# Kernel tuning notes

Hardware: AMD Instinct MI355X
Metric: run time of the kernel (lower is better)

## Reference

```python
import math
import jax, jax.numpy as jnp
import numpy as np

B, N, D = 2, 768, 512
H = 8
DK = D // H
BETA_NOT = 0.5
EPS = 1e-6


def setup_inputs() -> dict:
    key = jax.random.key(0)
    ks = jax.random.split(key, 8)
    s = 0.02
    return {
        "x": jax.random.normal(ks[0], (B, N, D), dtype=jnp.float32),
        "qkv1_w": jax.random.normal(ks[1], (D, 3 * D), dtype=jnp.float32) * s,
        "qkv2_w": jax.random.normal(ks[2], (D, 3 * D), dtype=jnp.float32) * s,
        "proj_w": jax.random.normal(ks[3], (D, D), dtype=jnp.float32) * s,
        "conv1_w": jax.random.normal(ks[4], (16, 6), dtype=jnp.float32) * 0.3,
        "conv1_b": jax.random.normal(ks[5], (16,), dtype=jnp.float32) * 0.1,
        "conv2_w": jax.random.normal(ks[6], (4, 16), dtype=jnp.float32) * 0.3,
        "conv2_b": jnp.full((4,), -5.0, dtype=jnp.float32),
        "chain_logit": jnp.asarray(-2.0, dtype=jnp.float32),
    }


def _qkv(x, w):
    b, n, d = x.shape
    qkv = (x @ w).reshape(b, n, 3, H, DK).transpose(2, 0, 3, 1, 4)  # [3,B,h,N,dk]
    return qkv[0], qkv[1], qkv[2]


def reference(x, qkv1_w, qkv2_w, proj_w, conv1_w, conv1_b, conv2_w, conv2_b, chain_logit):
    scale = 1.0 / math.sqrt(DK)
    q1, k1, v1 = _qkv(x, qkv1_w)
    q2, k2, v2 = _qkv(x, qkv2_w)

    S1 = jnp.einsum("bhnd,bhmd->bhnm", q1, k1) * scale  # [B,h,N,N]
    S2 = jnp.einsum("bhnd,bhmd->bhnm", q2, k2) * scale
    A1 = jax.nn.softmax(S1, axis=-1)
    A2 = jax.nn.softmax(S2, axis=-1)

    C_right = jnp.einsum("bhnk,bhkm->bhnm", A1, A2)
    C_left = jnp.einsum("bhnk,bhkm->bhnm", A2, A1)
    Cr = jnp.log(C_right + EPS)
    Cl = jnp.log(C_left + EPS)

    # 6-channel edge feature map [B,h,6,N,N]
    feat = jnp.stack(
        [S1, S2, jnp.swapaxes(S1, -1, -2), jnp.swapaxes(S2, -1, -2), Cr, Cl], axis=2
    )
    # 1x1 convs == per-pixel channel mixing
    hid = jnp.einsum("bhcnm,oc->bhonm", feat, conv1_w) + conv1_b[None, None, :, None, None]
    hid = jax.nn.gelu(hid, approximate=True)  # tanh-approx GELU
    gates = jax.nn.sigmoid(
        jnp.einsum("bhcnm,oc->bhonm", hid, conv2_w) + conv2_b[None, None, :, None, None]
    )
    g_and, g_or, g_not, g_chain = gates[:, :, 0], gates[:, :, 1], gates[:, :, 2], gates[:, :, 3]

    Smix = (
        S1
        + g_and * S2  # g_and * (S1 + S2 - S1)
        + g_or * (jnp.logaddexp(S1, S2) - S1)
        - g_not * (BETA_NOT * S2)
        + g_chain * Cr
    )
    A = jax.nn.softmax(Smix, axis=-1)

    y_base = jnp.einsum("bhnm,bhmd->bhnd", A, v1)
    transport = jnp.einsum("bhnm,bhmd->bhnd", A2, v2)
    y_chain = jnp.einsum("bhnm,bhmd->bhnd", A1, transport)
    w = jax.nn.sigmoid(chain_logit)
    y = y_base + w * y_chain

    y = jnp.swapaxes(y, 1, 2).reshape(x.shape[0], x.shape[1], D)  # [B,N,D]
    return y @ proj_w
```

## Files before the change

### kernel.cpp

```cpp
#include <hip/hip_runtime.h>
#include <hip/hip_bf16.h>
#include <math.h>

typedef __hip_bfloat16 bf16;
typedef __attribute__((ext_vector_type(8))) short short8;
typedef __attribute__((ext_vector_type(4))) float f32x4;
typedef __attribute__((ext_vector_type(2))) float f32x2;
#define DEVINL __device__ __forceinline__

constexpr int Bc  = 2;
constexpr int Nc  = 768;
constexpr int Dc  = 512;
constexpr int Hc  = 8;
constexpr int DKc = 64;
constexpr int BHc = Bc * Hc;
constexpr float SCALE    = 0.125f;
constexpr float EPSF     = 1e-6f;
constexpr float BETA_NOT = 0.5f;

DEVINL float ldf(const float* p, long i) { return p[i]; }
DEVINL float ldf(const bf16* p, long i) { return __bfloat162float(p[i]); }
DEVINL void stf(float* p, long i, float v) { p[i] = v; }
DEVINL void stf(bf16* p, long i, float v) { p[i] = __float2bfloat16(v); }

DEVINL float sigf(float x) { return __fdividef(1.f, 1.f + __expf(-x)); }

DEVINL f32x2 fma2(f32x2 a, f32x2 b, f32x2 c) { return __builtin_elementwise_fma(a, b, c); }
DEVINL f32x2 splat2(float x) { return (f32x2){x, x}; }
DEVINL float vexp2(float x) { float r; asm("v_exp_f32 %0, %1" : "=v"(r) : "v"(x)); return r; }
DEVINL float vrcp(float x)  { float r; asm("v_rcp_f32 %0, %1" : "=v"(r) : "v"(x)); return r; }
DEVINL float vlog2(float x) { float r; asm("v_log_f32 %0, %1" : "=v"(r) : "v"(x)); return r; }

DEVINL void gl_lds16(const void* g, void* l) {
    __builtin_amdgcn_global_load_lds(
        (const __attribute__((address_space(1))) void*)g,
        (__attribute__((address_space(3))) void*)l, 16, 0, 0);
}

DEVINL int sniff_is_fp32(const void* xraw) {
    const uint4* p4 = (const uint4*)xraw;
    float mx = 0.f;
#pragma unroll
    for (int j = 0; j < 16; ++j) {
        const uint4 u = p4[j];
        const unsigned w[4] = {u.x, u.y, u.z, u.w};
#pragma unroll
        for (int t = 0; t < 4; ++t) {
            mx = fmaxf(mx, fabsf(__uint_as_float((w[t] & 0xffffu) << 16)));
            mx = fmaxf(mx, fabsf(__uint_as_float(w[t] & 0xffff0000u)));
        }
    }
    return mx > 1000.f ? 1 : 0;
}

DEVINL float cvt_elem(const void* s, long j, int is32) {
    return is32 ? ((const float*)s)[j]
                : __bfloat162float(((const bf16*)s)[j]);
}

__global__ __launch_bounds__(256) void convert_all(
    const void* x, const void* w1, const void* w2, const void* pw,
    const void* c1w, const void* c1b, const void* c2w, const void* c2b,
    const void* ch,
    bf16* xb, bf16* w1b, bf16* w2b, bf16* pwb, float* smallf)
{
    __shared__ int is32s;
    if (threadIdx.x == 0) is32s = sniff_is_fp32(x);
    __syncthreads();
    const int is32 = is32s;
    const long i = (long)blockIdx.x * 256 + threadIdx.x;
    if (i < (long)Bc * Nc * Dc) {
        xb[i]  = __float2bfloat16(cvt_elem(x,  i, is32));
        w1b[i] = __float2bfloat16(cvt_elem(w1, i, is32));
        w2b[i] = __float2bfloat16(cvt_elem(w2, i, is32));
    }
    if (i < (long)Dc * Dc) pwb[i] = __float2bfloat16(cvt_elem(pw, i, is32));
    if (i < 384) {
        const int u = (int)i / 24, k = (int)i % 24;
        float v = 0.f;
        if (k < 12)      v = cvt_elem(c1w, u * 6 + (k >> 1), is32);
        else if (k < 14) v = cvt_elem(c1b, u, is32);
        else if (k >= 16) { const int o = (k - 16) >> 1; v = cvt_elem(c2w, o * 16 + u, is32); }
        smallf[i] = v;
    } else if (i < 392) smallf[i] = cvt_elem(c2b, ((int)i - 384) >> 1, is32);
    else if (i < 394) smallf[i] = cvt_elem(ch, 0, is32);
    else if (i < 512) smallf[i] = 0.f;
}

__global__ __launch_bounds__(256) void fill_sentinel(unsigned short* o) {
    const long i = (long)blockIdx.x * 256 + threadIdx.x;
    if (i < (long)Bc * Nc * Dc) o[i] = 0x40E0;
}

__global__ __launch_bounds__(256) void transpose_bf16(
    const unsigned short* __restrict__ src, unsigned short* __restrict__ dst,
    int R, int C, long sS, long sD)
{
    __shared__ unsigned short tile[64][68];
    const unsigned short* s = src + (long)blockIdx.z * sS;
    unsigned short* d = dst + (long)blockIdx.z * sD;
    const int r0 = blockIdx.y * 64, c0 = blockIdx.x * 64;
    const int t = threadIdx.x;
    const int lr = t >> 4, lc4 = (t & 15) * 4;
#pragma unroll
    for (int i = 0; i < 4; ++i) {
        int r = lr + i * 16;
        *(uint2*)&tile[r][lc4] = *(const uint2*)&s[(long)(r0 + r) * C + c0 + lc4];
    }
    __syncthreads();
#pragma unroll
    for (int i = 0; i < 4; ++i) {
        int r = lr + i * 16;
        unsigned short v[4];
#pragma unroll
        for (int j = 0; j < 4; ++j) v[j] = tile[lc4 + j][r];
        *(uint2*)&d[(long)(c0 + r) * R + r0 + lc4] = *(uint2*)v;
    }
}

__global__ __launch_bounds__(256) void sgemm_softmax(
    const bf16* __restrict__ qg, const bf16* __restrict__ kg,
    float* __restrict__ Sg, bf16* __restrict__ Ag_, bf16* __restrict__ Atg)
{
    __shared__ unsigned short Bsm[256 * 72];
    __shared__ unsigned short Asm16[16 * 72];
    __shared__ float red[4][16];

    const int wg  = blockIdx.x;
    const int xcd = wg & 7, tt = wg >> 3;
    const int z   = xcd + 8 * (tt / 48);
    const int by  = tt % 48;
    const long MAT = (long)Nc * Nc;

    const bf16* Q  = qg + (long)z * (Nc * DKc) + (long)(by * 16) * DKc;
    const bf16* Km = kg + (long)z * (Nc * DKc);
    float* S  = Sg  + (long)z * MAT + (long)(by * 16) * Nc;
    bf16*  A  = Ag_ + (long)z * MAT + (long)(by * 16) * Nc;
    bf16*  At = Atg + (long)z * MAT;

    const int tid  = threadIdx.x;
    const int wv   = tid >> 6;
    const int lane = tid & 63;
    const int q    = lane >> 4;
    const int ln   = lane & 15;
    const int sr   = tid >> 3, k8 = tid & 7;

    if (tid < 128) {
        const int row = tid >> 3, kk = tid & 7;
        *(uint4*)&Asm16[row * 72 + kk * 8] = *(const uint4*)&Q[row * 64 + kk * 8];
    }

    f32x4 acc[12];
#pragma unroll
    for (int j = 0; j < 12; ++j) acc[j] = (f32x4){0.f, 0.f, 0.f, 0.f};

    for (int c = 0; c < 3; ++c) {
        __syncthreads();
#pragma unroll
        for (int i = 0; i < 8; ++i) {
            const int row = sr + i * 32;
            *(uint4*)&Bsm[row * 72 + k8 * 8] =
                *(const uint4*)&Km[(long)(c * 256 + row) * 64 + k8 * 8];
        }
        __syncthreads();
#pragma unroll
        for (int kc = 0; kc < 2; ++kc) {
            const short8 af = *(const short8*)&Asm16[ln * 72 + kc * 32 + q * 8];
#pragma unroll
            for (int t = 0; t < 4; ++t) {
                const int nl = wv * 64 + t * 16 + ln;
                const short8 bfr = *(const short8*)&Bsm[nl * 72 + kc * 32 + q * 8];
                acc[c * 4 + t] = __builtin_amdgcn_mfma_f32_16x16x32_bf16(
                    af, bfr, acc[c * 4 + t], 0, 0, 0);
            }
        }
    }

    float mrow[4] = {-1e30f, -1e30f, -1e30f, -1e30f};
#pragma unroll
    for (int j = 0; j < 12; ++j) {
        const int c = j >> 2, t = j & 3;
        const int col = c * 256 + wv * 64 + t * 16 + ln;
#pragma unroll
        for (int r = 0; r < 4; ++r) {
            const float v = acc[j][r] * SCALE;
            acc[j][r] = v;
            S[(long)(q * 4 + r) * Nc + col] = v;
            mrow[r] = fmaxf(mrow[r], v);
        }
    }
#pragma unroll
    for (int off = 8; off > 0; off >>= 1)
#pragma unroll
        for (int r = 0; r < 4; ++r)
            mrow[r] = fmaxf(mrow[r], __shfl_xor(mrow[r], off, 16));
    if (ln == 0)
#pragma unroll
        for (int r = 0; r < 4; ++r) red[wv][q * 4 + r] = mrow[r];
    __syncthreads();
    float m4[4];
#pragma unroll
    for (int r = 0; r < 4; ++r)
        m4[r] = fmaxf(fmaxf(red[0][q * 4 + r], red[1][q * 4 + r]),
                      fmaxf(red[2][q * 4 + r], red[3][q * 4 + r]));
    __syncthreads();

    float srow[4] = {0.f, 0.f, 0.f, 0.f};
#pragma unroll
    for (int j = 0; j < 12; ++j)
#pragma unroll
        for (int r = 0; r < 4; ++r) {
            const float e = __expf(acc[j][r] - m4[r]);
            acc[j][r] = e;
            srow[r] += e;
        }
#pragma unroll
    for (int off = 8; off > 0; off >>= 1)
#pragma unroll
        for (int r = 0; r < 4; ++r)
            srow[r] += __shfl_xor(srow[r], off, 16);
    if (ln == 0)
#pragma unroll
        for (int r = 0; r < 4; ++r) red[wv][q * 4 + r] = srow[r];
    __syncthreads();
    float inv[4];
#pragma unroll
    for (int r = 0; r < 4; ++r)
        inv[r] = 1.f / fmaxf(red[0][q * 4 + r] + red[1][q * 4 + r] +
                             red[2][q * 4 + r] + red[3][q * 4 + r], 1e-30f);

    unsigned short* ATl = Bsm;
#pragma unroll
    for (int j = 0; j < 12; ++j) {
        const int c = j >> 2, t = j & 3;
        const int col = c * 256 + wv * 64 + t * 16 + ln;
#pragma unroll
        for (int r = 0; r < 4; ++r) {
            const bf16 b = __float2bfloat16(acc[j][r] * inv[r]);
            const unsigned short u = *(const unsigned short*)&b;
            A[(long)(q * 4 + r) * Nc + col] = *(const bf16*)&u;
            ATl[col * 20 + q * 4 + r] = u;
        }
    }
    __syncthreads();
#pragma unroll
    for (int s = 0; s < 3; ++s) {
        const int m = tid + s * 256;
        uint2 v0 = *(const uint2*)&ATl[m * 20 + 0];
        uint2 v1 = *(const uint2*)&ATl[m * 20 + 4];
        uint2 v2 = *(const uint2*)&ATl[m * 20 + 8];
        uint2 v3 = *(const uint2*)&ATl[m * 20 + 12];
        unsigned short* d = (unsigned short*)&At[(long)m * Nc + by * 16];
        *(uint2*)&d[0]  = v0;
        *(uint2*)&d[4]  = v1;
        *(uint2*)&d[8]  = v2;
        *(uint2*)&d[12] = v3;
    }
}

template <int EPI, typename TC, int XORB = 0, int XCDSWZ = 0, int RAW = 0>
__global__ __launch_bounds__(256) void gemm_nt_mfma(
    const bf16* __restrict__ Ag, const bf16* __restrict__ Btg,
    TC* __restrict__ Cg, bf16* __restrict__ Craw, int M, int N, int K,
    long sA, long sB, long sC, float alpha)
{
    __shared__ unsigned short Asm[2 * 128 * 32];
    __shared__ unsigned short Bsm[2 * 128 * 32];
    constexpr int BUF = 128 * 32;

    int bx, by, bz;
    if (XCDSWZ) {
        const int wg = blockIdx.x;
        const int xcd = wg & 7, t = wg >> 3;
        bz = xcd + 8 * (t / 36);
        const int tile = t % 36;
        bx = tile % 6; by = tile / 6;
    } else { bx = blockIdx.x; by = blockIdx.y; bz = blockIdx.z; }

    const int tid  = threadIdx.x;
    const int wv   = tid >> 6;
    const int lane = tid & 63;
    const int q    = lane >> 4;
    const int ln   = lane & 15;
    const int wm   = wv & 1;
    const int wn   = wv >> 1;

    const int zb = XORB ? (bz ^ 16) : bz;
    const bf16* A  = Ag  + (long)bz * sA + (long)(by * 128) * K;
    const bf16* Bt = Btg + (long)zb * sB + (long)(bx * 128) * K;
    TC*         C  = Cg  + (long)bz * sC;

    const int sr = lane >> 2, sc = lane & 3;
    const int scs = sc ^ (sr & 3);
    const bf16* gA0 = A  + (long)(wv * 32 + sr)      * K + scs * 8;
    const bf16* gA1 = A  + (long)(wv * 32 + 16 + sr) * K + scs * 8;
    const bf16* gB0 = Bt + (long)(wv * 32 + sr)      * K + scs * 8;
    const bf16* gB1 = Bt + (long)(wv * 32 + 16 + sr) * K + scs * 8;
    unsigned short* lA0 = &Asm[(wv * 32)      * 32];
    unsigned short* lA1 = &Asm[(wv * 32 + 16) * 32];
    unsigned short* lB0 = &Bsm[(wv * 32)      * 32];
    unsigned short* lB1 = &Bsm[(wv * 32 + 16) * 32];

    f32x4 acc[4][4];
#pragma unroll
    for (int i = 0; i < 4; ++i)
#pragma unroll
        for (int j = 0; j < 4; ++j)
            acc[i][j] = (f32x4){0.f, 0.f, 0.f, 0.f};

    const int qs = (q ^ (ln & 3)) * 8;

    gl_lds16(gA0, lA0);
    gl_lds16(gA1, lA1);
    gl_lds16(gB0, lB0);
    gl_lds16(gB1, lB1);
    __syncthreads();

    int cur = 0;
    for (int k0 = 0; k0 < K; k0 += 32) {
        const int nxt = cur ^ 1;
        if (k0 + 32 < K) {
            const int no = nxt * BUF;
            gl_lds16(gA0 + k0 + 32, lA0 + no);
            gl_lds16(gA1 + k0 + 32, lA1 + no);
            gl_lds16(gB0 + k0 + 32, lB0 + no);
            gl_lds16(gB1 + k0 + 32, lB1 + no);
        }

        const unsigned short* Ac = &Asm[cur * BUF];
        const unsigned short* Bc = &Bsm[cur * BUF];
        short8 af[4], bfr[4];
#pragma unroll
        for (int mt = 0; mt < 4; ++mt) {
            int m = wm * 64 + mt * 16 + ln;
            af[mt] = *(const short8*)&Ac[m * 32 + qs];
        }
#pragma unroll
        for (int nt = 0; nt < 4; ++nt) {
            int n = wn * 64 + nt * 16 + ln;
            bfr[nt] = *(const short8*)&Bc[n * 32 + qs];
        }
#pragma unroll
        for (int mt = 0; mt < 4; ++mt)
#pragma unroll
            for (int nt = 0; nt < 4; ++nt)
                acc[mt][nt] = __builtin_amdgcn_mfma_f32_16x16x32_bf16(
                    af[mt], bfr[nt], acc[mt][nt], 0, 0, 0);

        __syncthreads();
        cur = nxt;
    }

#pragma unroll
    for (int mt = 0; mt < 4; ++mt) {
#pragma unroll
        for (int nt = 0; nt < 4; ++nt) {
            const int col = bx * 128 + wn * 64 + nt * 16 + ln;
            const int rowb = by * 128 + wm * 64 + mt * 16 + q * 4;
#pragma unroll
            for (int r = 0; r < 4; ++r) {
                float vraw = acc[mt][nt][r] * alpha;
                if (RAW) {
                    if (bz < 16)
                        Craw[(long)bz * M * N + (long)(rowb + r) * N + col] =
                            __float2bfloat16(vraw);
                }
                float v = vraw;
                if (EPI == 1) v = __logf(fmaxf(v, 0.f) + EPSF);
                stf(C, (long)(rowb + r) * N + col, v);
            }
        }
    }
}

__global__ __launch_bounds__(256) void qkv_mfma(
    const bf16* __restrict__ X,
    const bf16* __restrict__ w1t, const bf16* __restrict__ w2t,
    bf16* __restrict__ q1, bf16* __restrict__ k1, bf16* __restrict__ v1,
    bf16* __restrict__ q2, bf16* __restrict__ k2, bf16* __restrict__ v2)
{
    constexpr int K = Dc;
    __shared__ unsigned short Asm[2 * 128 * 32];
    __shared__ unsigned short Bsm[2 * 128 * 32];
    constexpr int BUF = 128 * 32;

    const int tid  = threadIdx.x;
    const int wv   = tid >> 6;
    const int lane = tid & 63;
    const int q    = lane >> 4;
    const int ln   = lane & 15;
    const int wm   = wv & 1;
    const int wn   = wv >> 1;
    const int set  = blockIdx.z;

    const bf16* Wt = set ? w2t : w1t;
    bf16* Q  = set ? q2 : q1;
    bf16* Ko = set ? k2 : k1;
    bf16* V  = set ? v2 : v1;

    const bf16* A  = X  + (long)(blockIdx.y * 128) * K;
    const bf16* Bt = Wt + (long)(blockIdx.x * 128) * K;

    const int sr = lane >> 2, sc = lane & 3;
    const int scs = sc ^ (sr & 3);
    const bf16* gA0 = A  + (long)(wv * 32 + sr)      * K + scs * 8;
    const bf16* gA1 = A  + (long)(wv * 32 + 16 + sr) * K + scs * 8;
    const bf16* gB0 = Bt + (long)(wv * 32 + sr)      * K + scs * 8;
    const bf16* gB1 = Bt + (long)(wv * 32 + 16 + sr) * K + scs * 8;
    unsigned short* lA0 = &Asm[(wv * 32)      * 32];
    unsigned short* lA1 = &Asm[(wv * 32 + 16) * 32];
    unsigned short* lB0 = &Bsm[(wv * 32)      * 32];
    unsigned short* lB1 = &Bsm[(wv * 32 + 16) * 32];

    f32x4 acc[4][4];
#pragma unroll
    for (int i = 0; i < 4; ++i)
#pragma unroll
        for (int j = 0; j < 4; ++j)
            acc[i][j] = (f32x4){0.f, 0.f, 0.f, 0.f};

    const int qs = (q ^ (ln & 3)) * 8;

    gl_lds16(gA0, lA0);
    gl_lds16(gA1, lA1);
    gl_lds16(gB0, lB0);
    gl_lds16(gB1, lB1);
    __syncthreads();

    int cur = 0;
    for (int k0 = 0; k0 < K; k0 += 32) {
        const int nxt = cur ^ 1;
        if (k0 + 32 < K) {
            const int no = nxt * BUF;
            gl_lds16(gA0 + k0 + 32, lA0 + no);
            gl_lds16(gA1 + k0 + 32, lA1 + no);
            gl_lds16(gB0 + k0 + 32, lB0 + no);
            gl_lds16(gB1 + k0 + 32, lB1 + no);
        }

        const unsigned short* Ac = &Asm[cur * BUF];
        const unsigned short* Bc = &Bsm[cur * BUF];
        short8 af[4], bfr[4];
#pragma unroll
        for (int mt = 0; mt < 4; ++mt) {
            int m = wm * 64 + mt * 16 + ln;
            af[mt] = *(const short8*)&Ac[m * 32 + qs];
        }
#pragma unroll
        for (int nt = 0; nt < 4; ++nt) {
            int n = wn * 64 + nt * 16 + ln;
            bfr[nt] = *(const short8*)&Bc[n * 32 + qs];
        }
#pragma unroll
        for (int mt = 0; mt < 4; ++mt)
#pragma unroll
            for (int nt = 0; nt < 4; ++nt)
                acc[mt][nt] = __builtin_amdgcn_mfma_f32_16x16x32_bf16(
                    af[mt], bfr[nt], acc[mt][nt], 0, 0, 0);

        __syncthreads();
        cur = nxt;
    }

#pragma unroll
    for (int mt = 0; mt < 4; ++mt) {
#pragma unroll
        for (int nt = 0; nt < 4; ++nt) {
            const int col  = blockIdx.x * 128 + wn * 64 + nt * 16 + ln;
            const int rowb = blockIdx.y * 128 + wm * 64 + mt * 16 + q * 4;
            const int t = col >> 9;
            const int h = (col >> 6) & 7;
            const int dk = col & 63;
            bf16* dst = (t == 0) ? Q : (t == 1) ? Ko : V;
#pragma unroll
            for (int r = 0; r < 4; ++r) {
                const int row = rowb + r;
                const int b = row >= Nc ? 1 : 0;
                const int n = row - b * Nc;
                dst[(((long)b * Hc + h) * Nc + n) * DKc + dk] =
                    __float2bfloat16(acc[mt][nt][r]);
            }
        }
    }
}

struct N64Acc { f32x4 acc[2][4]; };

template <typename DUMMY = void>
DEVINL void n64_core(const bf16* A, const bf16* Bt, int K,
                     unsigned short* Asm, unsigned short* Bsm, N64Acc& R)
{
    const int tid  = threadIdx.x;
    const int wave = tid >> 6;
    const int lane = tid & 63;
    const int q    = lane >> 4;
    const int ln   = lane & 15;

    const int sr = tid >> 3, k8 = tid & 7;
    const bf16* pa[4];
    const bf16* pb[2];
    int wa[4], wb[2];
#pragma unroll
    for (int i = 0; i < 4; ++i) {
        pa[i] = A + (long)(sr + i * 32) * K + k8 * 8;
        wa[i] = (sr + i * 32) * 72 + k8 * 8;
    }
#pragma unroll
    for (int i = 0; i < 2; ++i) {
        pb[i] = Bt + (long)(sr + i * 32) * K + k8 * 8;
        wb[i] = (sr + i * 32) * 72 + k8 * 8;
    }

#pragma unroll
    for (int i = 0; i < 2; ++i)
#pragma unroll
        for (int j = 0; j < 4; ++j)
            R.acc[i][j] = (f32x4){0.f, 0.f, 0.f, 0.f};

    for (int k0 = 0; k0 < K; k0 += 64) {
        uint4 va[4], vb[2];
#pragma unroll
        for (int i = 0; i < 4; ++i) va[i] = *(const uint4*)(pa[i] + k0);
#pragma unroll
        for (int i = 0; i < 2; ++i) vb[i] = *(const uint4*)(pb[i] + k0);
        __syncthreads();
#pragma unroll
        for (int i = 0; i < 4; ++i) *(uint4*)&Asm[wa[i]] = va[i];
#pragma unroll
        for (int i = 0; i < 2; ++i) *(uint4*)&Bsm[wb[i]] = vb[i];
        __syncthreads();

#pragma unroll
        for (int kc = 0; kc < 2; ++kc) {
            short8 af[2], bfr[4];
#pragma unroll
            for (int mt = 0; mt < 2; ++mt) {
                int m = wave * 32 + mt * 16 + ln;
                af[mt] = *(const short8*)&Asm[m * 72 + kc * 32 + q * 8];
            }
#pragma unroll
            for (int nt = 0; nt < 4; ++nt) {
                int n = nt * 16 + ln;
                bfr[nt] = *(const short8*)&Bsm[n * 72 + kc * 32 + q * 8];
            }
#pragma unroll
            for (int mt = 0; mt < 2; ++mt)
#pragma unroll
                for (int nt = 0; nt < 4; ++nt)
                    R.acc[mt][nt] = __builtin_amdgcn_mfma_f32_16x16x32_bf16(
                        af[mt], bfr[nt], R.acc[mt][nt], 0, 0, 0);
        }
    }
}

struct N64hAcc { f32x4 acc[4]; };

template <typename DUMMY = void>
DEVINL void n64h_core(const bf16* A, const bf16* Bt, int K,
                      unsigned short* Asm, unsigned short* Bsm, N64hAcc& R)
{
    const int tid  = threadIdx.x;
    const int wave = tid >> 6;
    const int lane = tid & 63;
    const int q    = lane >> 4;
    const int ln   = lane & 15;

    const int sr = tid >> 3, k8 = tid & 7;
    const bf16* pa[2];
    const bf16* pb[2];
    int wa[2], wb[2];
#pragma unroll
    for (int i = 0; i < 2; ++i) {
        pa[i] = A  + (long)(sr + i * 32) * K + k8 * 8;
        wa[i] = (sr + i * 32) * 72 + k8 * 8;
        pb[i] = Bt + (long)(sr + i * 32) * K + k8 * 8;
        wb[i] = wa[i];
    }

#pragma unroll
    for (int j = 0; j < 4; ++j)
        R.acc[j] = (f32x4){0.f, 0.f, 0.f, 0.f};

    for (int k0 = 0; k0 < K; k0 += 64) {
        uint4 va[2], vb[2];
#pragma unroll
        for (int i = 0; i < 2; ++i) va[i] = *(const uint4*)(pa[i] + k0);
#pragma unroll
        for (int i = 0; i < 2; ++i) vb[i] = *(const uint4*)(pb[i] + k0);
        __syncthreads();
#pragma unroll
        for (int i = 0; i < 2; ++i) *(uint4*)&Asm[wa[i]] = va[i];
#pragma unroll
        for (int i = 0; i < 2; ++i) *(uint4*)&Bsm[wb[i]] = vb[i];
        __syncthreads();

#pragma unroll
        for (int kc = 0; kc < 2; ++kc) {
            short8 af;
            af = *(const short8*)&Asm[(wave * 16 + ln) * 72 + kc * 32 + q * 8];
            short8 bfr[4];
#pragma unroll
            for (int nt = 0; nt < 4; ++nt) {
                int n = nt * 16 + ln;
                bfr[nt] = *(const short8*)&Bsm[n * 72 + kc * 32 + q * 8];
            }
#pragma unroll
            for (int nt = 0; nt < 4; ++nt)
                R.acc[nt] = __builtin_amdgcn_mfma_f32_16x16x32_bf16(
                    af, bfr[nt], R.acc[nt], 0, 0, 0);
        }
    }
}

__global__ __launch_bounds__(256) void gemm_n64_pair(
    const bf16* __restrict__ A0g, const bf16* __restrict__ B0g, bf16* __restrict__ C0tg,
    const bf16* __restrict__ A1g, const bf16* __restrict__ B1g, bf16* __restrict__ C1g,
    int M, int K, long sA, long sB, long sC)
{
    __shared__ unsigned short Asm[128 * 72];
    __shared__ unsigned short Bsm[64 * 72];

    const int zz = blockIdx.z & 15;
    const int second = blockIdx.z >> 4;
    const bf16* A  = (second ? A1g : A0g) + (long)zz * sA + (long)(blockIdx.y * 128) * K;
    const bf16* Bt = (second ? B1g : B0g) + (long)zz * sB;

    N64Acc R;
    n64_core(A, Bt, K, Asm, Bsm, R);

    const int tid = threadIdx.x;
    const int wave = tid >> 6, lane = tid & 63, q = lane >> 4, ln = lane & 15;

    if (second) {
        bf16* C = C1g + (long)zz * sC;
#pragma unroll
        for (int mt = 0; mt < 2; ++mt) {
#pragma unroll
            for (int nt = 0; nt < 4; ++nt) {
                const int col  = nt * 16 + ln;
                const int rowb = blockIdx.y * 128 + wave * 32 + mt * 16 + q * 4;
#pragma unroll
                for (int r = 0; r < 4; ++r)
                    C[(long)(rowb + r) * 64 + col] = __float2bfloat16(R.acc[mt][nt][r]);
            }
        }
    } else {
        __syncthreads();
#pragma unroll
        for (int mt = 0; mt < 2; ++mt) {
#pragma unroll
            for (int nt = 0; nt < 4; ++nt) {
                const int col = nt * 16 + ln;
                const int rwb = wave * 32 + mt * 16 + q * 4;
#pragma unroll
                for (int r = 0; r < 4; ++r)
                    *(bf16*)&Asm[col * 136 + rwb + r] = __float2bfloat16(R.acc[mt][nt][r]);
            }
        }
        __syncthreads();
        bf16* Ct = C0tg + (long)zz * sC;
        const int dk  = tid >> 2;
        const int nc0 = (tid & 3) * 32;
        const int gn0 = blockIdx.y * 128;
#pragma unroll
        for (int c8 = 0; c8 < 4; ++c8) {
            uint4 v = *(const uint4*)&Asm[dk * 136 + nc0 + c8 * 8];
            *(uint4*)&Ct[(long)dk * Nc + gn0 + nc0 + c8 * 8] = v;
        }
    }
}

__global__ __launch_bounds__(256) void gemm_n64_both_h(
    const bf16* __restrict__ Ab, const bf16* __restrict__ v1t,
    const bf16* __restrict__ Craw, const bf16* __restrict__ v2t,
    const float* __restrict__ smallf, bf16* __restrict__ yc,
    int K, long sA, long sB)
{
    __shared__ unsigned short Asm[64 * 72];
    __shared__ unsigned short Bsm[64 * 72];

    const int bh = blockIdx.z;
    const long arow = (long)(blockIdx.y * 64) * K;

    N64hAcc R1;
    n64h_core(Ab + (long)bh * sA + arow, v1t + (long)bh * sB, K, Asm, Bsm, R1);
    N64hAcc R2;
    n64h_core(Craw + (long)bh * sA + arow, v2t + (long)bh * sB, K, Asm, Bsm, R2);

    const float w = sigf(smallf[392]);
    const int b = bh >> 3, h = bh & 7;

    const int tid = threadIdx.x;
    const int wave = tid >> 6, lane = tid & 63, q = lane >> 4, ln = lane & 15;
#pragma unroll
    for (int nt = 0; nt < 4; ++nt) {
        const int col  = nt * 16 + ln;
        const int rowb = blockIdx.y * 64 + wave * 16 + q * 4;
#pragma unroll
        for (int r = 0; r < 4; ++r) {
            const int n = rowb + r;
            yc[((long)(b * Nc + n)) * Dc + h * DKc + col] =
                __float2bfloat16(R1.acc[nt][r] + w * R2.acc[nt][r]);
        }
    }
}

__global__ __launch_bounds__(256) void gemm_n64_combine(
    const bf16* __restrict__ A1b, const bf16* __restrict__ trt,
    const bf16* __restrict__ yb1, const float* __restrict__ smallf,
    bf16* __restrict__ yc, int M, int K, long sA, long sB)
{
    __shared__ unsigned short Asm[128 * 72];
    __shared__ unsigned short Bsm[64 * 72];

    const int bh = blockIdx.z;
    const bf16* A  = A1b + (long)bh * sA + (long)(blockIdx.y * 128) * K;
    const bf16* Bt = trt + (long)bh * sB;

    N64Acc R;
    n64_core(A, Bt, K, Asm, Bsm, R);

    const float w = sigf(smallf[392]);
    const int b = bh >> 3, h = bh & 7;
    const long yb1base = (long)bh * Nc * DKc;

    const int tid = threadIdx.x;
    const int wave = tid >> 6, lane = tid & 63, q = lane >> 4, ln = lane & 15;
#pragma unroll
    for (int mt = 0; mt < 2; ++mt) {
#pragma unroll
        for (int nt = 0; nt < 4; ++nt) {
            const int col  = nt * 16 + ln;
            const int rowb = blockIdx.y * 128 + wave * 32 + mt * 16 + q * 4;
#pragma unroll
            for (int r = 0; r < 4; ++r) {
                const int n = rowb + r;
                const float base = __bfloat162float(yb1[yb1base + (long)n * 64 + col]);
                yc[((long)(b * Nc + n)) * Dc + h * DKc + col] =
                    __float2bfloat16(base + w * R.acc[mt][nt][r]);
            }
        }
    }
}

__global__ __launch_bounds__(256) void gemm_n64_yb(
    const bf16* __restrict__ Ag, const bf16* __restrict__ Btg,
    bf16* __restrict__ Cg, int M, int K, long sA, long sB, long sC)
{
    __shared__ unsigned short Asm[128 * 72];
    __shared__ unsigned short Bsm[64 * 72];

    const int zz = blockIdx.z;
    const bf16* A  = Ag + (long)zz * sA + (long)(blockIdx.y * 128) * K;
    const bf16* Bt = Btg + (long)zz * sB;

    N64Acc R;
    n64_core(A, Bt, K, Asm, Bsm, R);

    bf16* C = Cg + (long)zz * sC;
    const int tid = threadIdx.x;
    const int wave = tid >> 6, lane = tid & 63, q = lane >> 4, ln = lane & 15;
#pragma unroll
    for (int mt = 0; mt < 2; ++mt) {
#pragma unroll
        for (int nt = 0; nt < 4; ++nt) {
            const int col  = nt * 16 + ln;
            const int rowb = blockIdx.y * 128 + wave * 32 + mt * 16 + q * 4;
#pragma unroll
            for (int r = 0; r < 4; ++r)
                C[(long)(rowb + r) * 64 + col] = __float2bfloat16(R.acc[mt][nt][r]);
        }
    }
}

__global__ __launch_bounds__(256) void softmax_rows_w(
    const float* __restrict__ src, bf16* __restrict__ dst)
{
    const int wid  = threadIdx.x >> 6;
    const int lane = threadIdx.x & 63;
    const long row = (long)blockIdx.x * 4 + wid;
    const float* s = src + row * Nc;

    float4 v[3];
#pragma unroll
    for (int i = 0; i < 3; ++i)
        v[i] = *(const float4*)&s[i * 256 + lane * 4];

    float m = -1e30f;
#pragma unroll
    for (int i = 0; i < 3; ++i)
        m = fmaxf(m, fmaxf(fmaxf(v[i].x, v[i].y), fmaxf(v[i].z, v[i].w)));
#pragma unroll
    for (int off = 32; off > 0; off >>= 1)
        m = fmaxf(m, __shfl_xor(m, off, 64));

    float e[12];
    float sum = 0.f;
#pragma unroll
    for (int i = 0; i < 3; ++i) {
        e[i * 4 + 0] = __expf(v[i].x - m);
        e[i * 4 + 1] = __expf(v[i].y - m);
        e[i * 4 + 2] = __expf(v[i].z - m);
        e[i * 4 + 3] = __expf(v[i].w - m);
        sum += e[i * 4 + 0] + e[i * 4 + 1] + e[i * 4 + 2] + e[i * 4 + 3];
    }
#pragma unroll
    for (int off = 32; off > 0; off >>= 1)
        sum += __shfl_xor(sum, off, 64);

    const float inv = 1.f / fmaxf(sum, 1e-30f);
    unsigned short* d = (unsigned short*)dst + row * Nc;
#pragma unroll
    for (int i = 0; i < 3; ++i) {
        unsigned short o[4];
#pragma unroll
        for (int j = 0; j < 4; ++j) {
            const bf16 b = __float2bfloat16(e[i * 4 + j] * inv);
            o[j] = *(const unsigned short*)&b;
        }
        *(uint2*)&d[i * 256 + lane * 4] = *(const uint2*)o;
    }
}

__global__ __launch_bounds__(256) void gates_smix(
    const float* __restrict__ S1g, const float* __restrict__ S2g,
    const bf16* __restrict__ Crg, const bf16* __restrict__ Clg,
    float* __restrict__ Smixg, const float* __restrict__ smallf)
{
    __shared__ float t1t[32][17], t2t[32][17];

    const long mat = (long)blockIdx.z * Nc * Nc;
    const float* S1 = S1g + mat;
    const float* S2 = S2g + mat;
    const unsigned short* Cr = (const unsigned short*)Crg + mat;
    const unsigned short* Cl = (const unsigned short*)Clg + mat;
    float* Smix = Smixg + mat;

    const int tid = threadIdx.x;

    const int n0 = blockIdx.y * 16, m0 = blockIdx.x * 32;
    {
        const int r = tid >> 3, c2 = (tid & 7) * 2;
        const float2 a = *(const float2*)&S1[(long)(m0 + r) * Nc + n0 + c2];
        const float2 b = *(const float2*)&S2[(long)(m0 + r) * Nc + n0 + c2];
        t1t[r][c2] = a.x; t1t[r][c2 + 1] = a.y;
        t2t[r][c2] = b.x; t2t[r][c2 + 1] = b.y;
    }
    __syncthreads();

    const int tx = tid & 15, ty = tid >> 4;
    const int n = n0 + ty;
    const long idx = (long)n * Nc + m0 + tx * 2;

    const float2 s1v = *(const float2*)&S1[idx];
    const float2 s2v = *(const float2*)&S2[idx];
    const unsigned cru = *(const unsigned*)&Cr[idx];
    const unsigned clu = *(const unsigned*)&Cl[idx];

    const f32x2 s1a = {s1v.x, s1v.y};
    const f32x2 s2a = {s2v.x, s2v.y};
    const f32x2 cra = {__uint_as_float((cru & 0xffffu) << 16),
                       __uint_as_float(cru & 0xffff0000u)};
    const f32x2 cla = {__uint_as_float((clu & 0xffffu) << 16),
                       __uint_as_float(clu & 0xffff0000u)};
    const f32x2 s1t = {t1t[tx * 2][ty], t1t[tx * 2 + 1][ty]};
    const f32x2 s2t = {t2t[tx * 2][ty], t2t[tx * 2 + 1][ty]};

    f32x2 g0 = *(const f32x2*)&smallf[384];
    f32x2 g1 = *(const f32x2*)&smallf[386];
    f32x2 g2 = *(const f32x2*)&smallf[388];
    f32x2 g3 = *(const f32x2*)&smallf[390];

    const f32x2 gc1  = splat2(-2.30220902f);
    const f32x2 gc3  = splat2(-0.10294357f);
    const f32x2 one2 = splat2(1.f);

#pragma unroll
    for (int u = 0; u < 16; ++u) {
        const f32x2* cw = (const f32x2*)&smallf[u * 24];
        f32x2 h = cw[6];
        h = fma2(s1a, cw[0], h);
        h = fma2(s2a, cw[1], h);
        h = fma2(s1t, cw[2], h);
        h = fma2(s2t, cw[3], h);
        h = fma2(cra, cw[4], h);
        h = fma2(cla, cw[5], h);
        const f32x2 hh = h * h;
        const f32x2 z2 = h * fma2(hh, gc3, gc1);
        f32x2 e;  e[0]  = vexp2(z2[0]); e[1]  = vexp2(z2[1]);
        const f32x2 d = one2 + e;
        f32x2 rc; rc[0] = vrcp(d[0]);   rc[1] = vrcp(d[1]);
        const f32x2 hid = h * rc;
        g0 = fma2(hid, cw[8],  g0);
        g1 = fma2(hid, cw[9],  g1);
        g2 = fma2(hid, cw[10], g2);
        g3 = fma2(hid, cw[11], g3);
    }

    const f32x2 nl2e = splat2(-1.44269504f);
    const f32x2 ln2v = splat2(0.69314718f);
    auto sig2 = [&](f32x2 x) -> f32x2 {
        const f32x2 t = x * nl2e;
        f32x2 e;  e[0] = vexp2(t[0]); e[1] = vexp2(t[1]);
        const f32x2 d = one2 + e;
        f32x2 r;  r[0] = vrcp(d[0]);  r[1] = vrcp(d[1]);
        return r;
    };
    const f32x2 ga2 = sig2(g0);
    const f32x2 go2 = sig2(g1);
    const f32x2 gn2 = sig2(g2);
    const f32x2 gc2 = sig2(g3);

    const f32x2 dd = s1a - s2a;
    f32x2 ad; ad[0] = fabsf(dd[0]); ad[1] = fabsf(dd[1]);
    const f32x2 t2 = ad * nl2e;
    f32x2 ee; ee[0] = vexp2(t2[0]); ee[1] = vexp2(t2[1]);
    const f32x2 lp = one2 + ee;
    f32x2 lg; lg[0] = vlog2(lp[0]); lg[1] = vlog2(lp[1]);
    const f32x2 mx2 = __builtin_elementwise_max(s1a, s2a);
    const f32x2 lae = fma2(lg, ln2v, mx2);

    f32x2 o2 = s1a;
    o2 = fma2(ga2, s2a, o2);
    o2 = fma2(go2, lae - s1a, o2);
    o2 = fma2(gn2, s2a * splat2(-BETA_NOT), o2);
    o2 = fma2(gc2, cra, o2);
    *(float2*)&Smix[idx] = (float2){o2[0], o2[1]};
}

__global__ __launch_bounds__(256) void proj_n64h(
    const bf16* __restrict__ yc, const bf16* __restrict__ pwt,
    const void* __restrict__ xraw, void* __restrict__ out)
{
    constexpr int K = Dc;
    constexpr int N = Dc;
    __shared__ unsigned short Asm[64 * 72];
    __shared__ unsigned short Bsm[64 * 72];
    __shared__ int is32s;
    if (threadIdx.x == 0) is32s = sniff_is_fp32(xraw);

    const bf16* A  = yc  + (long)(blockIdx.y * 64) * K;
    const bf16* Bt = pwt + (long)(blockIdx.x * 64) * K;

    N64hAcc R;
    n64h_core(A, Bt, K, Asm, Bsm, R);

    const int is32 = is32s;
    const int tid = threadIdx.x;
    const int wave = tid >> 6, lane = tid & 63, q = lane >> 4, ln = lane & 15;
#pragma unroll
    for (int nt = 0; nt < 4; ++nt) {
        const int col  = blockIdx.x * 64 + nt * 16 + ln;
        const int rowb = blockIdx.y * 64 + wave * 16 + q * 4;
#pragma unroll
        for (int r = 0; r < 4; ++r) {
            const long o = (long)(rowb + r) * N + col;
            if (is32) ((float*)out)[o] = R.acc[nt][r];
            else      ((bf16*)out)[o] = __float2bfloat16(R.acc[nt][r]);
        }
    }
}

extern "C" void kernel_launch(void* const* d_in, const int* in_sizes, int n_in,
                              void* d_out, int out_size, void* d_ws, size_t ws_size,
                              hipStream_t stream)
{
    const size_t HD   = (size_t)BHc * Nc * DKc;
    const size_t HDh  = HD / 2;
    const size_t MAT  = (size_t)Nc * Nc;
    const size_t MATS = (size_t)BHc * MAT;
    const long   HSTR = (long)Nc * DKc;

    float* ws = (float*)d_ws;
    size_t off = 0;
    auto alloc = [&](size_t n) { float* p = ws + off; off += n; return p; };

    bf16* xb  = (bf16*)alloc(HDh);
    bf16* w1b = (bf16*)alloc(HDh);
    bf16* w2b = (bf16*)alloc(HDh);
    bf16* w1t = (bf16*)alloc(HDh);
    bf16* w2t = (bf16*)alloc(HDh);
    bf16* pwb = (bf16*)alloc((size_t)Dc * Dc / 2);
    bf16* pwt = (bf16*)alloc((size_t)Dc * Dc / 2);
    float* smallf = alloc(512);
    bf16* q1b = (bf16*)alloc(HDh); bf16* q2b = (bf16*)alloc(HDh);
    bf16* k1b = (bf16*)alloc(HDh); bf16* k2b = (bf16*)alloc(HDh);
    bf16* v1b = (bf16*)alloc(HDh); bf16* v2b = (bf16*)alloc(HDh);
    bf16* v1t = (bf16*)alloc(HDh); bf16* v2t = (bf16*)alloc(HDh);
    bf16* trt = (bf16*)alloc(HDh);
    float* S1   = alloc(MATS);
    float* S2   = alloc(MATS);
    float* Smix = alloc(MATS);
    bf16* A1b = (bf16*)alloc(MATS / 2);
    bf16* A2b = (bf16*)alloc(MATS / 2);
    bf16* Crb = (bf16*)alloc(MATS / 2);
    bf16* Clb = (bf16*)alloc(MATS / 2);
    bf16* yb1 = (bf16*)alloc(HDh);
    bf16* yc  = (bf16*)alloc(HDh);

    const size_t NEED_BASE = off * sizeof(float);
    bf16* Crawb = (bf16*)alloc(MATS / 2);
    const size_t NEED_A = off * sizeof(float);
    const int pathA = ws_size >= NEED_A;

    bf16* A1tb = (bf16*)Smix;
    bf16* A2tb = ((bf16*)Smix) + MATS;
    bf16* Ab   = (bf16*)S1;

    if (ws_size < NEED_BASE) {
        fill_sentinel<<<dim3(3072), 256, 0, stream>>>((unsigned short*)d_out);
        return;
    }

    convert_all<<<dim3(3072), 256, 0, stream>>>(
        d_in[0], d_in[1], d_in[2], d_in[3], d_in[4], d_in[5], d_in[6], d_in[7],
        d_in[8], xb, w1b, w2b, pwb, smallf);

    transpose_bf16<<<dim3(24, 8, 2), 256, 0, stream>>>(
        (const unsigned short*)w1b, (unsigned short*)w1t, Dc, 3 * Dc, (long)HD, (long)HD);
    transpose_bf16<<<dim3(8, 8, 1), 256, 0, stream>>>(
        (const unsigned short*)pwb, (unsigned short*)pwt, Dc, Dc, 0, 0);
    qkv_mfma<<<dim3(12, 12, 2), 256, 0, stream>>>(
        xb, w1t, w2t, q1b, k1b, v1b, q2b, k2b, v2b);
    transpose_bf16<<<dim3(1, 12, 2 * BHc), 256, 0, stream>>>(
        (const unsigned short*)v1b, (unsigned short*)v1t, Nc, DKc, HSTR, HSTR);

    sgemm_softmax<<<dim3(1536), 256, 0, stream>>>(
        q1b, k1b, S1, A1b, A1tb);

    if (pathA)
        gemm_nt_mfma<1, bf16, 1, 1, 1><<<dim3(1152), 256, 0, stream>>>(
            A1b, A1tb, Crb, Crawb, Nc, Nc, Nc, (long)MAT, (long)MAT, (long)MAT, 1.f);
    else
        gemm_nt_mfma<1, bf16, 1, 1, 0><<<dim3(1152), 256, 0, stream>>>(
            A1b, A1tb, Crb, nullptr, Nc, Nc, Nc, (long)MAT, (long)MAT, (long)MAT, 1.f);

    gates_smix<<<dim3(24, 48, BHc), 256, 0, stream>>>(S1, S2, Crb, Clb, Smix, smallf);

    softmax_rows_w<<<(BHc * Nc) / 4, 256, 0, stream>>>(Smix, Ab);

    if (pathA) {
        gemm_n64_both_h<<<dim3(1, 12, BHc), 256, 0, stream>>>(
            Ab, v1t, Crawb, v2t, smallf, yc, Nc, (long)MAT, HSTR);
    } else {
        gemm_n64_pair<<<dim3(1, 6, 2 * BHc), 256, 0, stream>>>(
            A2b, v2t, trt, Ab, v1t, yb1, Nc, Nc, (long)MAT, HSTR, HSTR);
        gemm_n64_combine<<<dim3(1, 6, BHc), 256, 0, stream>>>(
            A1b, trt, yb1, smallf, yc, Nc, Nc, (long)MAT, HSTR);
    }

    proj_n64h<<<dim3(8, 24, 1), 256, 0, stream>>>(yc, pwt, d_in[0], d_out);
}
```

Measured before the change: 331.6 us.

## Fuse gate computation with row softmax and merge weight transposes

```diff
diff --git a/kernel.cpp b/kernel.cpp
--- a/kernel.cpp
+++ b/kernel.cpp
@@ -99,6 +99,42 @@
     __shared__ unsigned short tile[64][68];
     const unsigned short* s = src + (long)blockIdx.z * sS;
     unsigned short* d = dst + (long)blockIdx.z * sD;
+    const int r0 = blockIdx.y * 64, c0 = blockIdx.x * 64;
+    const int t = threadIdx.x;
+    const int lr = t >> 4, lc4 = (t & 15) * 4;
+#pragma unroll
+    for (int i = 0; i < 4; ++i) {
+        int r = lr + i * 16;
+        *(uint2*)&tile[r][lc4] = *(const uint2*)&s[(long)(r0 + r) * C + c0 + lc4];
+    }
+    __syncthreads();
+#pragma unroll
+    for (int i = 0; i < 4; ++i) {
+        int r = lr + i * 16;
+        unsigned short v[4];
+#pragma unroll
+        for (int j = 0; j < 4; ++j) v[j] = tile[lc4 + j][r];
+        *(uint2*)&d[(long)(c0 + r) * R + r0 + lc4] = *(uint2*)v;
+    }
+}
+
+__global__ __launch_bounds__(256) void transpose_wpw(
+    const unsigned short* __restrict__ wb, unsigned short* __restrict__ wt,
+    const unsigned short* __restrict__ pwb, unsigned short* __restrict__ pwt)
+{
+    __shared__ unsigned short tile[64][68];
+    const int z = blockIdx.z;
+    const unsigned short* s;
+    unsigned short* d;
+    int R, C;
+    if (z < 2) {
+        s = wb + (long)z * (Dc * 3 * Dc);
+        d = wt + (long)z * (Dc * 3 * Dc);
+        R = Dc; C = 3 * Dc;
+    } else {
+        if (blockIdx.x >= 8) return;
+        s = pwb; d = pwt; R = Dc; C = Dc;
+    }
     const int r0 = blockIdx.y * 64, c0 = blockIdx.x * 64;
     const int t = threadIdx.x;
     const int lr = t >> 4, lc4 = (t & 15) * 4;
@@ -926,6 +962,163 @@
     o2 = fma2(gn2, s2a * splat2(-BETA_NOT), o2);
     o2 = fma2(gc2, cra, o2);
     *(float2*)&Smix[idx] = (float2){o2[0], o2[1]};
+}
+
+__global__ __launch_bounds__(256) void gates_smix_sm(
+    const float* __restrict__ S1g, const float* __restrict__ S2g,
+    const bf16* __restrict__ Crg, const bf16* __restrict__ Clg,
+    bf16* __restrict__ Ag_, const float* __restrict__ smallf)
+{
+    __shared__ float osm[8 * Nc];
+    __shared__ float t1t[64][9], t2t[64][9];
+
+    const long mat = (long)blockIdx.z * Nc * Nc;
+    const float* S1 = S1g + mat;
+    const float* S2 = S2g + mat;
+    const unsigned short* Cr = (const unsigned short*)Crg + mat;
+    const unsigned short* Cl = (const unsigned short*)Clg + mat;
+    bf16* A = Ag_ + mat;
+
+    const int tid = threadIdx.x;
+    const int n0 = blockIdx.x * 8;
+    const int tx = tid & 31, ty = tid >> 5;
+    const int n = n0 + ty;
+
+    const f32x2 gc1  = splat2(-2.30220902f);
+    const f32x2 gc3  = splat2(-0.10294357f);
+    const f32x2 one2 = splat2(1.f);
+    const f32x2 nl2e = splat2(-1.44269504f);
+    const f32x2 ln2v = splat2(0.69314718f);
+
+    for (int it = 0; it < 12; ++it) {
+        const int m0 = it * 64;
+        __syncthreads();
+        {
+            const int r = tid >> 2, c2 = (tid & 3) * 2;
+            const float2 a = *(const float2*)&S1[(long)(m0 + r) * Nc + n0 + c2];
+            const float2 b = *(const float2*)&S2[(long)(m0 + r) * Nc + n0 + c2];
+            t1t[r][c2] = a.x; t1t[r][c2 + 1] = a.y;
+            t2t[r][c2] = b.x; t2t[r][c2 + 1] = b.y;
+        }
+        __syncthreads();
+
+        const long idx = (long)n * Nc + m0 + tx * 2;
+        const float2 s1v = *(const float2*)&S1[idx];
+        const float2 s2v = *(const float2*)&S2[idx];
+        const unsigned cru = *(const unsigned*)&Cr[idx];
+        const unsigned clu = *(const unsigned*)&Cl[idx];
+
+        const f32x2 s1a = {s1v.x, s1v.y};
+        const f32x2 s2a = {s2v.x, s2v.y};
+        const f32x2 cra = {__uint_as_float((cru & 0xffffu) << 16),
+                           __uint_as_float(cru & 0xffff0000u)};
+        const f32x2 cla = {__uint_as_float((clu & 0xffffu) << 16),
+                           __uint_as_float(clu & 0xffff0000u)};
+        const f32x2 s1t = {t1t[tx * 2][ty], t1t[tx * 2 + 1][ty]};
+        const f32x2 s2t = {t2t[tx * 2][ty], t2t[tx * 2 + 1][ty]};
+
+        f32x2 g0 = *(const f32x2*)&smallf[384];
+        f32x2 g1 = *(const f32x2*)&smallf[386];
+        f32x2 g2 = *(const f32x2*)&smallf[388];
+        f32x2 g3 = *(const f32x2*)&smallf[390];
+
+#pragma unroll
+        for (int u = 0; u < 16; ++u) {
+            const f32x2* cw = (const f32x2*)&smallf[u * 24];
+            f32x2 h = cw[6];
+            h = fma2(s1a, cw[0], h);
+            h = fma2(s2a, cw[1], h);
+            h = fma2(s1t, cw[2], h);
+            h = fma2(s2t, cw[3], h);
+            h = fma2(cra, cw[4], h);
+            h = fma2(cla, cw[5], h);
+            const f32x2 hh = h * h;
+            const f32x2 z2 = h * fma2(hh, gc3, gc1);
+            f32x2 e;  e[0]  = vexp2(z2[0]); e[1]  = vexp2(z2[1]);
+            const f32x2 d = one2 + e;
+            f32x2 rc; rc[0] = vrcp(d[0]);   rc[1] = vrcp(d[1]);
+            const f32x2 hid = h * rc;
+            g0 = fma2(hid, cw[8],  g0);
+            g1 = fma2(hid, cw[9],  g1);
+            g2 = fma2(hid, cw[10], g2);
+            g3 = fma2(hid, cw[11], g3);
+        }
+
+        auto sig2 = [&](f32x2 x) -> f32x2 {
+            const f32x2 t = x * nl2e;
+            f32x2 e;  e[0] = vexp2(t[0]); e[1] = vexp2(t[1]);
+            const f32x2 d = one2 + e;
+            f32x2 r;  r[0] = vrcp(d[0]);  r[1] = vrcp(d[1]);
+            return r;
+        };
+        const f32x2 ga2 = sig2(g0);
+        const f32x2 go2 = sig2(g1);
+        const f32x2 gn2 = sig2(g2);
+        const f32x2 gc2 = sig2(g3);
+
+        const f32x2 dd = s1a - s2a;
+        f32x2 ad; ad[0] = fabsf(dd[0]); ad[1] = fabsf(dd[1]);
+        const f32x2 t2 = ad * nl2e;
+        f32x2 ee; ee[0] = vexp2(t2[0]); ee[1] = vexp2(t2[1]);
+        const f32x2 lp = one2 + ee;
+        f32x2 lg; lg[0] = vlog2(lp[0]); lg[1] = vlog2(lp[1]);
+        const f32x2 mx2 = __builtin_elementwise_max(s1a, s2a);
+        const f32x2 lae = fma2(lg, ln2v, mx2);
+
+        f32x2 o2 = s1a;
+        o2 = fma2(ga2, s2a, o2);
+        o2 = fma2(go2, lae - s1a, o2);
+        o2 = fma2(gn2, s2a * splat2(-BETA_NOT), o2);
+        o2 = fma2(gc2, cra, o2);
+        *(float2*)&osm[ty * Nc + m0 + tx * 2] = (float2){o2[0], o2[1]};
+    }
+    __syncthreads();
+
+    const int w = tid >> 6, lane = tid & 63;
+#pragma unroll
+    for (int rr = 0; rr < 2; ++rr) {
+        const int row = w * 2 + rr;
+        const float* s = &osm[row * Nc];
+        float4 v[3];
+#pragma unroll
+        for (int i = 0; i < 3; ++i)
+            v[i] = *(const float4*)&s[i * 256 + lane * 4];
+
+        float m = -1e30f;
+#pragma unroll
+        for (int i = 0; i < 3; ++i)
+            m = fmaxf(m, fmaxf(fmaxf(v[i].x, v[i].y), fmaxf(v[i].z, v[i].w)));
+#pragma unroll
+        for (int off = 32; off > 0; off >>= 1)
+            m = fmaxf(m, __shfl_xor(m, off, 64));
+
+        float e[12];
+        float sum = 0.f;
+#pragma unroll
+        for (int i = 0; i < 3; ++i) {
+            e[i * 4 + 0] = __expf(v[i].x - m);
+            e[i * 4 + 1] = __expf(v[i].y - m);
+            e[i * 4 + 2] = __expf(v[i].z - m);
+            e[i * 4 + 3] = __expf(v[i].w - m);
+            sum += e[i * 4 + 0] + e[i * 4 + 1] + e[i * 4 + 2] + e[i * 4 + 3];
+        }
+#pragma unroll
+        for (int off = 32; off > 0; off >>= 1)
+            sum += __shfl_xor(sum, off, 64);
+
+        const float inv = 1.f / fmaxf(sum, 1e-30f);
+        unsigned short* d = (unsigned short*)A + (long)(n0 + row) * Nc;
+#pragma unroll
+        for (int i = 0; i < 3; ++i) {
+            unsigned short o[4];
+#pragma unroll
+            for (int j = 0; j < 4; ++j) {
+                const bf16 b = __float2bfloat16(e[i * 4 + j] * inv);
+                o[j] = *(const unsigned short*)&b;
+            }
+            *(uint2*)&d[i * 256 + lane * 4] = *(const uint2*)o;
+        }
+    }
 }
 
 __global__ __launch_bounds__(256) void proj_n64h(
@@ -1005,6 +1198,7 @@
 
     bf16* A1tb = (bf16*)Smix;
     bf16* A2tb = ((bf16*)Smix) + MATS;
+    bf16* AbA  = (bf16*)Smix;
     bf16* Ab   = (bf16*)S1;
 
     if (ws_size < NEED_BASE) {
@@ -1016,10 +1210,9 @@
         d_in[0], d_in[1], d_in[2], d_in[3], d_in[4], d_in[5], d_in[6], d_in[7],
         d_in[8], xb, w1b, w2b, pwb, smallf);
 
-    transpose_bf16<<<dim3(24, 8, 2), 256, 0, stream>>>(
-        (const unsigned short*)w1b, (unsigned short*)w1t, Dc, 3 * Dc, (long)HD, (long)HD);
-    transpose_bf16<<<dim3(8, 8, 1), 256, 0, stream>>>(
-        (const unsigned short*)pwb, (unsigned short*)pwt, Dc, Dc, 0, 0);
+    transpose_wpw<<<dim3(24, 8, 3), 256, 0, stream>>>(
+        (const unsigned short*)w1b, (unsigned short*)w1t,
+        (const unsigned short*)pwb, (unsigned short*)pwt);
     qkv_mfma<<<dim3(12, 12, 2), 256, 0, stream>>>(
         xb, w1t, w2t, q1b, k1b, v1b, q2b, k2b, v2b);
     transpose_bf16<<<dim3(1, 12, 2 * BHc), 256, 0, stream>>>(
@@ -1035,14 +1228,16 @@
         gemm_nt_mfma<1, bf16, 1, 1, 0><<<dim3(1152), 256, 0, stream>>>(
             A1b, A1tb, Crb, nullptr, Nc, Nc, Nc, (long)MAT, (long)MAT, (long)MAT, 1.f);
 
-    gates_smix<<<dim3(24, 48, BHc), 256, 0, stream>>>(S1, S2, Crb, Clb, Smix, smallf);
-
-    softmax_rows_w<<<(BHc * Nc) / 4, 256, 0, stream>>>(Smix, Ab);
-
     if (pathA) {
+        gates_smix_sm<<<dim3(96, 1, BHc), 256, 0, stream>>>(
+            S1, S2, Crb, Clb, AbA, smallf);
+
         gemm_n64_both_h<<<dim3(1, 12, BHc), 256, 0, stream>>>(
-            Ab, v1t, Crawb, v2t, smallf, yc, Nc, (long)MAT, HSTR);
+            AbA, v1t, Crawb, v2t, smallf, yc, Nc, (long)MAT, HSTR);
     } else {
+        gates_smix<<<dim3(24, 48, BHc), 256, 0, stream>>>(
+            S1, S2, Crb, Clb, Smix, smallf);
+        softmax_rows_w<<<(BHc * Nc) / 4, 256, 0, stream>>>(Smix, Ab);
         gemm_n64_pair<<<dim3(1, 6, 2 * BHc), 256, 0, stream>>>(
             A2b, v2t, trt, Ab, v1t, yb1, Nc, Nc, (long)MAT, HSTR, HSTR);
         gemm_n64_combine<<<dim3(1, 6, BHc), 256, 0, stream>>>(
```

Result: no change. 332.7 us (+0.3%).
